# Kernel tuning notes

Measured on AMD Instinct MI355X. Metric: run time of the kernel, lower is better.

The kernel has to match this reference:

```python
import jax, jax.numpy as jnp
import numpy as np

N_NODES = 10000
AVG_DEG = 32
N_FEAT = 512
HIDDEN = 32
CODE = 16


def setup_inputs() -> dict:
    key = jax.random.key(0)
    k1, k2, k3, k4, k5 = jax.random.split(key, 5)
    E = N_NODES * AVG_DEG
    src = jax.random.randint(k1, (E,), 0, N_NODES, dtype=jnp.int32)
    dst = jax.random.randint(k2, (E,), 0, N_NODES, dtype=jnp.int32)
    # A + I: add self loops (Kipf & Welling transform)
    loop = jnp.arange(N_NODES, dtype=jnp.int32)
    src = jnp.concatenate([src, loop])
    dst = jnp.concatenate([dst, loop])
    ones = jnp.ones(src.shape[0], jnp.float32)
    deg_row = jax.ops.segment_sum(ones, dst, num_segments=N_NODES)
    deg_col = jax.ops.segment_sum(ones, src, num_segments=N_NODES)
    # symmetric normalization D^-1/2 (A+I) D^-1/2
    edge_weight = jax.lax.rsqrt(deg_row[dst] * deg_col[src])
    x = jax.random.normal(k3, (N_NODES, N_FEAT), dtype=jnp.float32)
    W1 = jax.random.normal(k4, (N_FEAT, HIDDEN), dtype=jnp.float32) * 0.1
    W2 = jax.random.normal(k5, (HIDDEN, CODE), dtype=jnp.float32) * 0.1
    return {"x": x, "W1": W1, "W2": W2, "edge_weight": edge_weight,
            "src": src, "dst": dst}


def _spmm(edge_weight, src, dst, X):
    # sparse A_hat @ X via gather + weighted scatter-add
    return jax.ops.segment_sum(edge_weight[:, None] * X[src], dst,
                               num_segments=X.shape[0])


def reference(x, W1, W2, edge_weight, src, dst):
    # layer 1: A_hat @ (x @ W1), relu  (dropout inactive: eval mode)
    h = jax.nn.relu(_spmm(edge_weight, src, dst, x @ W1))
    # layer 2 (encoder): A_hat @ (h @ W2)
    z = _spmm(edge_weight, src, dst, h @ W2)  # [N, code]
    # inner-product decoder: sigmoid(Z Z^T)
    return jax.nn.sigmoid(jnp.einsum('nc,mc->nm', z, z))
```

## Files before the change

### kernel.cpp

```cpp
#include <hip/hip_runtime.h>
#include <hip/hip_bf16.h>

#define N_NODES 10000
#define N_FEAT  512
#define HIDDEN  32
#define CODE    16

typedef __attribute__((ext_vector_type(8))) short  short8;
typedef __attribute__((ext_vector_type(4))) float  floatx4;

__device__ __forceinline__ float bf2f(unsigned short h) {
    return __uint_as_float(((unsigned int)h) << 16);
}
__device__ __forceinline__ unsigned short f2bf(float f) {
    unsigned int u = __float_as_uint(f);
    u += 0x7fffu + ((u >> 16) & 1u);
    return (unsigned short)(u >> 16);
}
__device__ __forceinline__ float load_f(const void* p, size_t i, int isf32) {
    return isf32 ? ((const float*)p)[i] : bf2f(((const unsigned short*)p)[i]);
}
__device__ __forceinline__ int get_idx(const int* p, int e, int is64) {
    return is64 ? p[2 * (size_t)e] : p[e];
}

__global__ __launch_bounds__(384) void k_detect(const unsigned short* __restrict__ t0,
                                                const unsigned short* __restrict__ t1,
                                                const unsigned short* __restrict__ t2,
                                                const unsigned short* __restrict__ t3,
                                                const int* __restrict__ i0,
                                                const int* __restrict__ i1,
                                                int* __restrict__ flags) {
    const int w    = threadIdx.x >> 6;
    const int lane = threadIdx.x & 63;
    unsigned int m = 0;
    if (w < 4) {
        const unsigned short* p = (w == 0) ? t0 : (w == 1) ? t1 : (w == 2) ? t2 : t3;
        for (int i = lane; i < 128; i += 64) {
            unsigned int v = (unsigned int)p[2 * i] & 0x7fffu;
            m = m > v ? m : v;
        }
    } else {
        const int* p = (w == 4) ? i0 : i1;
        for (int i = lane; i < 128; i += 64) {
            m |= (unsigned int)p[2 * i + 1];
        }
    }
#pragma unroll
    for (int off = 32; off > 0; off >>= 1) {
        unsigned int o = (unsigned int)__shfl_down((int)m, off, 64);
        m = (w < 4) ? (m > o ? m : o) : (m | o);
    }
    if (lane == 0) flags[w] = (w < 4) ? (m >= 0x5000u ? 1 : 0) : (m == 0u ? 1 : 0);
}

__global__ __launch_bounds__(256) void k_xw1(const void* __restrict__ x,
                                             const void* __restrict__ W1,
                                             float* __restrict__ XW1,
                                             const int* __restrict__ flags) {
    const int xf32  = flags[0];
    const int w1f32 = flags[1];
    int t = blockIdx.x * 256 + threadIdx.x;
    if (t >= N_NODES * HIDDEN) return;
    const int n = t >> 5;
    const int c = t & 31;

    if (xf32 && w1f32) {
        const float* xr = (const float*)x + (size_t)n * N_FEAT;
        const float* w1 = (const float*)W1;
        float acc = 0.f;
#pragma unroll 4
        for (int k = 0; k < N_FEAT; k += 4) {
            floatx4 xa = *(const floatx4*)(xr + k);
            acc += xa[0] * w1[(k + 0) * HIDDEN + c];
            acc += xa[1] * w1[(k + 1) * HIDDEN + c];
            acc += xa[2] * w1[(k + 2) * HIDDEN + c];
            acc += xa[3] * w1[(k + 3) * HIDDEN + c];
        }
        XW1[t] = acc;
        return;
    }

    float acc = 0.f;
#pragma unroll 8
    for (int k = 0; k < N_FEAT; ++k) {
        float a = load_f(x,  (size_t)n * N_FEAT + k, xf32);
        float b = load_f(W1, (size_t)k * HIDDEN + c, w1f32);
        acc += a * b;
    }
    XW1[t] = acc;
}

__global__ __launch_bounds__(256) void k_spmm32(const void* __restrict__ ew,
                                                const int* __restrict__ src,
                                                const int* __restrict__ dst,
                                                const float* __restrict__ Xin,
                                                float* __restrict__ Hacc, int E,
                                                const int* __restrict__ flags) {
    const int ewf32 = flags[3];
    const int s64   = flags[4];
    const int d64   = flags[5];
    int t = blockIdx.x * 256 + threadIdx.x;
    int e = t >> 5;
    int f = t & 31;
    if (e >= E) return;
    float w = load_f(ew, e, ewf32);
    int   s = get_idx(src, e, s64);
    int   d = get_idx(dst, e, d64);
    float v = Xin[(size_t)s * HIDDEN + f] * w;
    atomicAdd(&Hacc[(size_t)d * HIDDEN + f], v);
}

__global__ __launch_bounds__(256) void k_hw2(const float* __restrict__ H,
                                             const void* __restrict__ W2,
                                             float* __restrict__ HW2,
                                             const int* __restrict__ flags) {
    const int w2f32 = flags[2];
    int t = blockIdx.x * 256 + threadIdx.x;
    if (t >= N_NODES * CODE) return;
    int n = t >> 4;
    int c = t & 15;
    float acc = 0.f;
#pragma unroll
    for (int k = 0; k < HIDDEN; ++k) {
        float h = H[n * HIDDEN + k];
        h = h > 0.f ? h : 0.f;
        acc += h * load_f(W2, k * CODE + c, w2f32);
    }
    HW2[t] = acc;
}

__global__ __launch_bounds__(256) void k_spmm16(const void* __restrict__ ew,
                                                const int* __restrict__ src,
                                                const int* __restrict__ dst,
                                                const float* __restrict__ Hin,
                                                float* __restrict__ Zacc, int E,
                                                const int* __restrict__ flags) {
    const int ewf32 = flags[3];
    const int s64   = flags[4];
    const int d64   = flags[5];
    int t = blockIdx.x * 256 + threadIdx.x;
    int e = t >> 4;
    int f = t & 15;
    if (e >= E) return;
    float w = load_f(ew, e, ewf32);
    int   s = get_idx(src, e, s64);
    int   d = get_idx(dst, e, d64);
    float v = Hin[(size_t)s * CODE + f] * w;
    atomicAdd(&Zacc[(size_t)d * CODE + f], v);
}

__global__ __launch_bounds__(256) void k_cvt(const float* __restrict__ Z,
                                             unsigned short* __restrict__ zb) {
    int t = blockIdx.x * 256 + threadIdx.x;
    if (t >= N_NODES * CODE) return;
    zb[t] = f2bf(Z[t]);
}

#define TLD 68

__global__ __launch_bounds__(256) void k_dec(const unsigned short* __restrict__ zb,
                                             float* __restrict__ out) {
    __shared__ float tile[64 * TLD];

    const int wave = threadIdx.x >> 6;
    const int lane = threadIdx.x & 63;
    const int l16  = lane & 15;
    const int quad = lane >> 4;

    const int rblk = blockIdx.y * 64;
    const int cblk = blockIdx.x * 64;
    const int r0   = rblk + wave * 16;

    const short8 zero8 = {0, 0, 0, 0, 0, 0, 0, 0};

    int ra = r0 + l16;
    if (ra > N_NODES - 1) ra = N_NODES - 1;
    short8 afr = zero8;
    if (quad < 2) afr = *(const short8*)(zb + (size_t)ra * CODE + quad * 8);

#pragma unroll
    for (int t = 0; t < 4; ++t) {
        int cb = cblk + t * 16 + l16;
        if (cb > N_NODES - 1) cb = N_NODES - 1;
        short8 bfr = zero8;
        if (quad < 2) bfr = *(const short8*)(zb + (size_t)cb * CODE + quad * 8);
        floatx4 z4 = {0.f, 0.f, 0.f, 0.f};
        floatx4 acc = __builtin_amdgcn_mfma_f32_16x16x32_bf16(afr, bfr, z4, 0, 0, 0);
        const int lrow = wave * 16 + quad * 4;
        const int lcol = t * 16 + l16;
#pragma unroll
        for (int r = 0; r < 4; ++r) {
            tile[(lrow + r) * TLD + lcol] = acc[r];
        }
    }
    __syncthreads();

    const int drow = threadIdx.x >> 4;
    const int dcol = (threadIdx.x & 15) * 4;
#pragma unroll
    for (int p = 0; p < 4; ++p) {
        const int lr = p * 16 + drow;
        floatx4 v;
#pragma unroll
        for (int j = 0; j < 4; ++j) {
            float s = tile[lr * TLD + dcol + j];
            float e = __builtin_amdgcn_exp2f(-1.442695041f * s);
            v[j] = __builtin_amdgcn_rcpf(1.f + e);
        }
        const int grow = rblk + lr;
        const int gcol = cblk + dcol;
        if (grow < N_NODES && gcol < N_NODES) {
            __builtin_nontemporal_store(v, (floatx4*)(out + (size_t)grow * N_NODES + gcol));
        }
    }
}

extern "C" void kernel_launch(void* const* d_in, const int* in_sizes, int n_in,
                              void* d_out, int out_size, void* d_ws, size_t ws_size,
                              hipStream_t stream) {
    const void* x  = d_in[0];
    const void* W1 = d_in[1];
    const void* W2 = d_in[2];
    const void* ew = d_in[3];
    const int* src = (const int*)d_in[4];
    const int* dst = (const int*)d_in[5];
    float* out = (float*)d_out;
    const int E = in_sizes[3];

    float* ws   = (float*)d_ws;
    float* XW1  = ws;
    float* Hacc = ws + 320000;
    float* HW2  = ws;
    float* Zacc = ws + 160000;
    unsigned short* zb = (unsigned short*)(ws + 320000);
    int* flags = (int*)(ws + 640000);

    hipMemsetAsync(Hacc, 0, 320000 * sizeof(float), stream);

    k_detect<<<1, 384, 0, stream>>>((const unsigned short*)x,
                                    (const unsigned short*)W1,
                                    (const unsigned short*)W2,
                                    (const unsigned short*)ew,
                                    src, dst, flags);

    k_xw1<<<(N_NODES * HIDDEN + 255) / 256, 256, 0, stream>>>(x, W1, XW1, flags);
    k_spmm32<<<(E * 32 + 255) / 256, 256, 0, stream>>>(ew, src, dst, XW1, Hacc, E, flags);
    hipMemsetAsync(Zacc, 0, 160000 * sizeof(float), stream);
    k_hw2<<<(N_NODES * CODE + 255) / 256, 256, 0, stream>>>(Hacc, W2, HW2, flags);
    k_spmm16<<<(E * 16 + 255) / 256, 256, 0, stream>>>(ew, src, dst, HW2, Zacc, E, flags);
    k_cvt<<<(N_NODES * CODE + 255) / 256, 256, 0, stream>>>(Zacc, zb);

    dim3 grid((N_NODES + 63) / 64, (N_NODES + 63) / 64);
    k_dec<<<grid, 256, 0, stream>>>(zb, out);
}
```

Baseline: 528.0 us.

## Build CSR by destination and replace atomic scatter SpMM with per-node gathers

Each call builds a CSR index of edges grouped by destination, using a histogram, a single-block scan and an atomic fill. Both SpMM layers then become per-node gather-reduce kernels with no float atomics, and the second layer writes bf16 z directly, removing the separate conversion kernel and both memsets. This trades about 330k float atomics per feature for three extra build kernels, one of which is a serial single-block scan. The path runs only if the workspace is large enough, otherwise the old atomic path is used.

```diff
diff --git a/kernel.cpp b/kernel.cpp
--- a/kernel.cpp
+++ b/kernel.cpp
@@ -91,6 +91,121 @@
     XW1[t] = acc;
 }
 
+__global__ __launch_bounds__(256) void k_hist(const int* __restrict__ dst,
+                                              int* __restrict__ deg, int E,
+                                              const int* __restrict__ flags) {
+    const int d64 = flags[5];
+    int e = blockIdx.x * 256 + threadIdx.x;
+    if (e >= E) return;
+    atomicAdd(&deg[get_idx(dst, e, d64)], 1);
+}
+
+__global__ __launch_bounds__(256) void k_scan(const int* __restrict__ deg,
+                                              int* __restrict__ rowptr, int E) {
+    __shared__ int parts[256];
+    const int t    = threadIdx.x;
+    const int base = t * 40;
+    int s = 0;
+#pragma unroll 8
+    for (int i = 0; i < 40; ++i) {
+        int idx = base + i;
+        if (idx < N_NODES) s += deg[idx];
+    }
+    parts[t] = s;
+    __syncthreads();
+    if (t == 0) {
+        int run = 0;
+        for (int i = 0; i < 256; ++i) { int v = parts[i]; parts[i] = run; run += v; }
+    }
+    __syncthreads();
+    int run = parts[t];
+    for (int i = 0; i < 40; ++i) {
+        int idx = base + i;
+        if (idx < N_NODES) { rowptr[idx] = run; run += deg[idx]; }
+    }
+    if (t == 255) rowptr[N_NODES] = E;
+}
+
+__global__ __launch_bounds__(256) void k_fill(const int* __restrict__ dst,
+                                              const int* __restrict__ rowptr,
+                                              int* __restrict__ cursor,
+                                              int* __restrict__ eidx, int E,
+                                              const int* __restrict__ flags) {
+    const int d64 = flags[5];
+    int e = blockIdx.x * 256 + threadIdx.x;
+    if (e >= E) return;
+    int d   = get_idx(dst, e, d64);
+    int pos = rowptr[d] + atomicAdd(&cursor[d], 1);
+    eidx[pos] = e;
+}
+
+__global__ __launch_bounds__(256) void k_gather32(const void* __restrict__ ew,
+                                                  const int* __restrict__ src,
+                                                  const int* __restrict__ rowptr,
+                                                  const int* __restrict__ eidx,
+                                                  const float* __restrict__ Xin,
+                                                  float* __restrict__ H,
+                                                  const int* __restrict__ flags) {
+    const int ewf32 = flags[3];
+    const int s64   = flags[4];
+    int t = blockIdx.x * 256 + threadIdx.x;
+    int node = t >> 5;
+    int f    = t & 31;
+    if (node >= N_NODES) return;
+    int p = rowptr[node], pe = rowptr[node + 1];
+    float acc = 0.f;
+    for (; p < pe; ++p) {
+        int   e = eidx[p];
+        float w = load_f(ew, e, ewf32);
+        int   s = get_idx(src, e, s64);
+        acc += w * Xin[(size_t)s * HIDDEN + f];
+    }
+    H[(size_t)node * HIDDEN + f] = acc;
+}
+
+__global__ __launch_bounds__(256) void k_hw2(const float* __restrict__ H,
+                                             const void* __restrict__ W2,
+                                             float* __restrict__ HW2,
+                                             const int* __restrict__ flags) {
+    const int w2f32 = flags[2];
+    int t = blockIdx.x * 256 + threadIdx.x;
+    if (t >= N_NODES * CODE) return;
+    int n = t >> 4;
+    int c = t & 15;
+    float acc = 0.f;
+#pragma unroll
+    for (int k = 0; k < HIDDEN; ++k) {
+        float h = H[n * HIDDEN + k];
+        h = h > 0.f ? h : 0.f;
+        acc += h * load_f(W2, k * CODE + c, w2f32);
+    }
+    HW2[t] = acc;
+}
+
+__global__ __launch_bounds__(256) void k_gather16(const void* __restrict__ ew,
+                                                  const int* __restrict__ src,
+                                                  const int* __restrict__ rowptr,
+                                                  const int* __restrict__ eidx,
+                                                  const float* __restrict__ Hin,
+                                                  unsigned short* __restrict__ zb,
+                                                  const int* __restrict__ flags) {
+    const int ewf32 = flags[3];
+    const int s64   = flags[4];
+    int t = blockIdx.x * 256 + threadIdx.x;
+    int node = t >> 4;
+    int f    = t & 15;
+    if (node >= N_NODES) return;
+    int p = rowptr[node], pe = rowptr[node + 1];
+    float acc = 0.f;
+    for (; p < pe; ++p) {
+        int   e = eidx[p];
+        float w = load_f(ew, e, ewf32);
+        int   s = get_idx(src, e, s64);
+        acc += w * Hin[(size_t)s * CODE + f];
+    }
+    zb[(size_t)node * CODE + f] = f2bf(acc);
+}
+
 __global__ __launch_bounds__(256) void k_spmm32(const void* __restrict__ ew,
                                                 const int* __restrict__ src,
                                                 const int* __restrict__ dst,
@@ -109,25 +224,6 @@
     int   d = get_idx(dst, e, d64);
     float v = Xin[(size_t)s * HIDDEN + f] * w;
     atomicAdd(&Hacc[(size_t)d * HIDDEN + f], v);
-}
-
-__global__ __launch_bounds__(256) void k_hw2(const float* __restrict__ H,
-                                             const void* __restrict__ W2,
-                                             float* __restrict__ HW2,
-                                             const int* __restrict__ flags) {
-    const int w2f32 = flags[2];
-    int t = blockIdx.x * 256 + threadIdx.x;
-    if (t >= N_NODES * CODE) return;
-    int n = t >> 4;
-    int c = t & 15;
-    float acc = 0.f;
-#pragma unroll
-    for (int k = 0; k < HIDDEN; ++k) {
-        float h = H[n * HIDDEN + k];
-        h = h > 0.f ? h : 0.f;
-        acc += h * load_f(W2, k * CODE + c, w2f32);
-    }
-    HW2[t] = acc;
 }
 
 __global__ __launch_bounds__(256) void k_spmm16(const void* __restrict__ ew,
@@ -229,14 +325,20 @@
     const int E = in_sizes[3];
 
     float* ws   = (float*)d_ws;
+    int*   wsi  = (int*)d_ws;
     float* XW1  = ws;
     float* Hacc = ws + 320000;
     float* HW2  = ws;
     float* Zacc = ws + 160000;
     unsigned short* zb = (unsigned short*)(ws + 320000);
-    int* flags = (int*)(ws + 640000);
-
-    hipMemsetAsync(Hacc, 0, 320000 * sizeof(float), stream);
+    int* flags  = wsi + 640000;
+    int* deg    = wsi + 640008;
+    int* cursor = wsi + 650008;
+    int* rowptr = wsi + 660008;
+    int* eidx   = wsi + 670016;
+
+    const size_t need_csr = (size_t)(670016 + E) * 4;
+    const int use_csr = (ws_size >= need_csr);
 
     k_detect<<<1, 384, 0, stream>>>((const unsigned short*)x,
                                     (const unsigned short*)W1,
@@ -244,12 +346,27 @@
                                     (const unsigned short*)ew,
                                     src, dst, flags);
 
-    k_xw1<<<(N_NODES * HIDDEN + 255) / 256, 256, 0, stream>>>(x, W1, XW1, flags);
-    k_spmm32<<<(E * 32 + 255) / 256, 256, 0, stream>>>(ew, src, dst, XW1, Hacc, E, flags);
-    hipMemsetAsync(Zacc, 0, 160000 * sizeof(float), stream);
-    k_hw2<<<(N_NODES * CODE + 255) / 256, 256, 0, stream>>>(Hacc, W2, HW2, flags);
-    k_spmm16<<<(E * 16 + 255) / 256, 256, 0, stream>>>(ew, src, dst, HW2, Zacc, E, flags);
-    k_cvt<<<(N_NODES * CODE + 255) / 256, 256, 0, stream>>>(Zacc, zb);
+    if (use_csr) {
+        hipMemsetAsync(deg, 0, 20000 * sizeof(int), stream);
+        k_hist<<<(E + 255) / 256, 256, 0, stream>>>(dst, deg, E, flags);
+        k_scan<<<1, 256, 0, stream>>>(deg, rowptr, E);
+        k_fill<<<(E + 255) / 256, 256, 0, stream>>>(dst, rowptr, cursor, eidx, E, flags);
+
+        k_xw1<<<(N_NODES * HIDDEN + 255) / 256, 256, 0, stream>>>(x, W1, XW1, flags);
+        k_gather32<<<(N_NODES * 32 + 255) / 256, 256, 0, stream>>>(ew, src, rowptr, eidx,
+                                                                   XW1, Hacc, flags);
+        k_hw2<<<(N_NODES * CODE + 255) / 256, 256, 0, stream>>>(Hacc, W2, HW2, flags);
+        k_gather16<<<(N_NODES * 16 + 255) / 256, 256, 0, stream>>>(ew, src, rowptr, eidx,
+                                                                   HW2, zb, flags);
+    } else {
+        hipMemsetAsync(Hacc, 0, 320000 * sizeof(float), stream);
+        k_xw1<<<(N_NODES * HIDDEN + 255) / 256, 256, 0, stream>>>(x, W1, XW1, flags);
+        k_spmm32<<<(E * 32 + 255) / 256, 256, 0, stream>>>(ew, src, dst, XW1, Hacc, E, flags);
+        hipMemsetAsync(Zacc, 0, 160000 * sizeof(float), stream);
+        k_hw2<<<(N_NODES * CODE + 255) / 256, 256, 0, stream>>>(Hacc, W2, HW2, flags);
+        k_spmm16<<<(E * 16 + 255) / 256, 256, 0, stream>>>(ew, src, dst, HW2, Zacc, E, flags);
+        k_cvt<<<(N_NODES * CODE + 255) / 256, 256, 0, stream>>>(Zacc, zb);
+    }
 
     dim3 grid((N_NODES + 63) / 64, (N_NODES + 63) / 64);
     k_dec<<<grid, 256, 0, stream>>>(zb, out);
```

New measurement: 609.0 us. 15.3% more time.

## Fuse accumulator zeroing, H@W2 projection, and bf16 conversion into neighboring kernels

Applied to the files above, without the earlier changes.

Zeroing of the Hacc and Zacc accumulators moves into the XW1 kernel whenever the workspace is large enough; otherwise the code falls back to memsets. The separate H@W2 kernel is removed: each edge thread in the second SpMM now computes relu(H[src]) @ W2 on the fly before its atomic add. The standalone bf16 conversion kernel is dropped, and the decoder converts fp32 Z fragments itself. This cuts several launches, memsets and intermediate buffers, at the cost of recomputing the 32-wide projection once per edge and converting fragments repeatedly in every decoder block.

```diff
diff --git a/kernel.cpp b/kernel.cpp
--- a/kernel.cpp
+++ b/kernel.cpp
@@ -57,11 +57,18 @@
 __global__ __launch_bounds__(256) void k_xw1(const void* __restrict__ x,
                                              const void* __restrict__ W1,
                                              float* __restrict__ XW1,
+                                             float* __restrict__ Hacc,
+                                             float* __restrict__ Zacc,
+                                             int zero_acc,
                                              const int* __restrict__ flags) {
     const int xf32  = flags[0];
     const int w1f32 = flags[1];
     int t = blockIdx.x * 256 + threadIdx.x;
     if (t >= N_NODES * HIDDEN) return;
+    if (zero_acc) {
+        Hacc[t] = 0.f;
+        if (t < N_NODES * CODE) Zacc[t] = 0.f;
+    }
     const int n = t >> 5;
     const int c = t & 31;
 
@@ -111,31 +118,14 @@
     atomicAdd(&Hacc[(size_t)d * HIDDEN + f], v);
 }
 
-__global__ __launch_bounds__(256) void k_hw2(const float* __restrict__ H,
-                                             const void* __restrict__ W2,
-                                             float* __restrict__ HW2,
-                                             const int* __restrict__ flags) {
+__global__ __launch_bounds__(256) void k_spmm16f(const void* __restrict__ ew,
+                                                 const int* __restrict__ src,
+                                                 const int* __restrict__ dst,
+                                                 const float* __restrict__ Hacc,
+                                                 const void* __restrict__ W2,
+                                                 float* __restrict__ Zacc, int E,
+                                                 const int* __restrict__ flags) {
     const int w2f32 = flags[2];
-    int t = blockIdx.x * 256 + threadIdx.x;
-    if (t >= N_NODES * CODE) return;
-    int n = t >> 4;
-    int c = t & 15;
-    float acc = 0.f;
-#pragma unroll
-    for (int k = 0; k < HIDDEN; ++k) {
-        float h = H[n * HIDDEN + k];
-        h = h > 0.f ? h : 0.f;
-        acc += h * load_f(W2, k * CODE + c, w2f32);
-    }
-    HW2[t] = acc;
-}
-
-__global__ __launch_bounds__(256) void k_spmm16(const void* __restrict__ ew,
-                                                const int* __restrict__ src,
-                                                const int* __restrict__ dst,
-                                                const float* __restrict__ Hin,
-                                                float* __restrict__ Zacc, int E,
-                                                const int* __restrict__ flags) {
     const int ewf32 = flags[3];
     const int s64   = flags[4];
     const int d64   = flags[5];
@@ -146,20 +136,33 @@
     float w = load_f(ew, e, ewf32);
     int   s = get_idx(src, e, s64);
     int   d = get_idx(dst, e, d64);
-    float v = Hin[(size_t)s * CODE + f] * w;
-    atomicAdd(&Zacc[(size_t)d * CODE + f], v);
-}
-
-__global__ __launch_bounds__(256) void k_cvt(const float* __restrict__ Z,
-                                             unsigned short* __restrict__ zb) {
-    int t = blockIdx.x * 256 + threadIdx.x;
-    if (t >= N_NODES * CODE) return;
-    zb[t] = f2bf(Z[t]);
+    const float* hr = Hacc + (size_t)s * HIDDEN;
+    float acc = 0.f;
+#pragma unroll
+    for (int k = 0; k < HIDDEN; ++k) {
+        float h = hr[k];
+        h = h > 0.f ? h : 0.f;
+        acc += h * load_f(W2, k * CODE + f, w2f32);
+    }
+    atomicAdd(&Zacc[(size_t)d * CODE + f], w * acc);
 }
 
 #define TLD 68
 
-__global__ __launch_bounds__(256) void k_dec(const unsigned short* __restrict__ zb,
+__device__ __forceinline__ short8 cvt_frag(const float* __restrict__ Z, int row, int quad) {
+    short8 r = {0, 0, 0, 0, 0, 0, 0, 0};
+    if (quad < 2) {
+        floatx4 a = *(const floatx4*)(Z + (size_t)row * CODE + quad * 8);
+        floatx4 b = *(const floatx4*)(Z + (size_t)row * CODE + quad * 8 + 4);
+        r[0] = (short)f2bf(a[0]); r[1] = (short)f2bf(a[1]);
+        r[2] = (short)f2bf(a[2]); r[3] = (short)f2bf(a[3]);
+        r[4] = (short)f2bf(b[0]); r[5] = (short)f2bf(b[1]);
+        r[6] = (short)f2bf(b[2]); r[7] = (short)f2bf(b[3]);
+    }
+    return r;
+}
+
+__global__ __launch_bounds__(256) void k_dec(const float* __restrict__ Z,
                                              float* __restrict__ out) {
     __shared__ float tile[64 * TLD];
 
@@ -172,19 +175,15 @@
     const int cblk = blockIdx.x * 64;
     const int r0   = rblk + wave * 16;
 
-    const short8 zero8 = {0, 0, 0, 0, 0, 0, 0, 0};
-
     int ra = r0 + l16;
     if (ra > N_NODES - 1) ra = N_NODES - 1;
-    short8 afr = zero8;
-    if (quad < 2) afr = *(const short8*)(zb + (size_t)ra * CODE + quad * 8);
+    short8 afr = cvt_frag(Z, ra, quad);
 
 #pragma unroll
     for (int t = 0; t < 4; ++t) {
         int cb = cblk + t * 16 + l16;
         if (cb > N_NODES - 1) cb = N_NODES - 1;
-        short8 bfr = zero8;
-        if (quad < 2) bfr = *(const short8*)(zb + (size_t)cb * CODE + quad * 8);
+        short8 bfr = cvt_frag(Z, cb, quad);
         floatx4 z4 = {0.f, 0.f, 0.f, 0.f};
         floatx4 acc = __builtin_amdgcn_mfma_f32_16x16x32_bf16(afr, bfr, z4, 0, 0, 0);
         const int lrow = wave * 16 + quad * 4;
@@ -231,12 +230,12 @@
     float* ws   = (float*)d_ws;
     float* XW1  = ws;
     float* Hacc = ws + 320000;
-    float* HW2  = ws;
-    float* Zacc = ws + 160000;
-    unsigned short* zb = (unsigned short*)(ws + 320000);
-    int* flags = (int*)(ws + 640000);
-
-    hipMemsetAsync(Hacc, 0, 320000 * sizeof(float), stream);
+
+    const size_t need_a = (size_t)(800006) * 4;
+    const int layout_a = (ws_size >= need_a);
+
+    float* Zacc = layout_a ? (ws + 640000) : (ws + 160000);
+    int*   flags = (int*)d_ws + (layout_a ? 800000 : 640000);
 
     k_detect<<<1, 384, 0, stream>>>((const unsigned short*)x,
                                     (const unsigned short*)W1,
@@ -244,13 +243,16 @@
                                     (const unsigned short*)ew,
                                     src, dst, flags);
 
-    k_xw1<<<(N_NODES * HIDDEN + 255) / 256, 256, 0, stream>>>(x, W1, XW1, flags);
+    if (!layout_a) {
+        hipMemsetAsync(Hacc, 0, 320000 * sizeof(float), stream);
+        hipMemsetAsync(Zacc, 0, 160000 * sizeof(float), stream);
+    }
+
+    k_xw1<<<(N_NODES * HIDDEN + 255) / 256, 256, 0, stream>>>(
+        x, W1, XW1, Hacc, Zacc, layout_a ? 1 : 0, flags);
     k_spmm32<<<(E * 32 + 255) / 256, 256, 0, stream>>>(ew, src, dst, XW1, Hacc, E, flags);
-    hipMemsetAsync(Zacc, 0, 160000 * sizeof(float), stream);
-    k_hw2<<<(N_NODES * CODE + 255) / 256, 256, 0, stream>>>(Hacc, W2, HW2, flags);
-    k_spmm16<<<(E * 16 + 255) / 256, 256, 0, stream>>>(ew, src, dst, HW2, Zacc, E, flags);
-    k_cvt<<<(N_NODES * CODE + 255) / 256, 256, 0, stream>>>(Zacc, zb);
+    k_spmm16f<<<(E * 16 + 255) / 256, 256, 0, stream>>>(ew, src, dst, Hacc, W2, Zacc, E, flags);
 
     dim3 grid((N_NODES + 63) / 64, (N_NODES + 63) / 64);
-    k_dec<<<grid, 256, 0, stream>>>(zb, out);
-}
+    k_dec<<<grid, 256, 0, stream>>>(Zacc, out);
+}
```

Result: slower. 544.6 us (+3.1%).
